# Optimization experiments

Hardware: AMD Instinct MI355X
Metric: run time of the kernel (lower is better)

## Reference

```python
import jax, jax.numpy as jnp
import numpy as np

N = 25600      # nodes
DEG = 16       # incoming edges per node
E = N * DEG    # 409600 edges
B = 8          # graphs in batch
F = 7          # node features
H = 300        # hidden_channels
L = 100        # latent_channels


def _mlp(h, W1, b1, W2, b2, W3, b3):
    h = jax.nn.relu(h @ W1 + b1)
    h = jax.nn.relu(h @ W2 + b2)
    return h @ W3 + b3


def _edge_layer(x, src, dst, params):
    # PyG MessagePassing(aggr='max'), flow source_to_target:
    # x_j = x[src] (edge_index[0]), x_i = x[dst] (edge_index[1])
    x_i = x[dst]
    x_j = x[src]
    m = _mlp(jnp.concatenate([x_i, x_j - x_i], axis=-1), *params)  # [E, out]
    # every node has >=1 incoming edge by construction, so no empty segments
    return jax.ops.segment_max(m, dst, num_segments=x.shape[0])


def setup_inputs() -> dict:
    key = jax.random.key(0)
    ks = jax.random.split(key, 24)
    x = jax.random.normal(ks[0], (N, F), jnp.float32)
    dst = jnp.repeat(jnp.arange(N, dtype=jnp.int32), DEG)          # every node covered
    src = jax.random.randint(ks[1], (E,), 0, N, dtype=jnp.int32)
    edge_index = jnp.stack([src, dst])                              # [2, E]
    batch = jnp.repeat(jnp.arange(B, dtype=jnp.int32), N // B)     # sorted graph ids

    def lin(k, i, o):
        return jax.random.normal(k, (i, o), jnp.float32) / jnp.sqrt(jnp.float32(i))

    def bias(k, o):
        return jax.random.normal(k, (o,), jnp.float32) * 0.01

    inp = dict(x=x, edge_index=edge_index, batch=batch)
    # layer 0 MLP: 2*F -> H -> H -> L
    inp.update(l0_W1=lin(ks[2], 2 * F, H), l0_b1=bias(ks[3], H),
               l0_W2=lin(ks[4], H, H),     l0_b2=bias(ks[5], H),
               l0_W3=lin(ks[6], H, L),     l0_b3=bias(ks[7], L))
    # layer 1 MLP: 2*L -> H -> H -> L
    inp.update(l1_W1=lin(ks[8], 2 * L, H), l1_b1=bias(ks[9], H),
               l1_W2=lin(ks[10], H, H),    l1_b2=bias(ks[11], H),
               l1_W3=lin(ks[12], H, L),    l1_b3=bias(ks[13], L))
    # final lin: 3*L -> L -> L -> 1
    inp.update(lin_W1=lin(ks[14], 3 * L, L), lin_b1=bias(ks[15], L),
               lin_W2=lin(ks[16], L, L),     lin_b2=bias(ks[17], L),
               lin_W3=lin(ks[18], L, 1),     lin_b3=bias(ks[19], 1))
    return inp


def reference(x, edge_index, batch,
              l0_W1, l0_b1, l0_W2, l0_b2, l0_W3, l0_b3,
              l1_W1, l1_b1, l1_W2, l1_b2, l1_W3, l1_b3,
              lin_W1, lin_b1, lin_W2, lin_b2, lin_W3, lin_b3):
    src, dst = edge_index[0], edge_index[1]
    h = _edge_layer(x, src, dst, (l0_W1, l0_b1, l0_W2, l0_b2, l0_W3, l0_b3))
    h = jax.nn.relu(h)
    h = _edge_layer(h, src, dst, (l1_W1, l1_b1, l1_W2, l1_b2, l1_W3, l1_b3))
    h = jax.nn.relu(h)                                              # [N, L]
    addp = jax.ops.segment_sum(h, batch, num_segments=B)
    cnt = jax.ops.segment_sum(jnp.ones((h.shape[0], 1), h.dtype), batch, num_segments=B)
    meanp = addp / cnt
    maxp = jax.ops.segment_max(h, batch, num_segments=B)
    pooled = jnp.concatenate([addp, meanp, maxp], axis=1)           # [B, 3L]
    return _mlp(pooled, lin_W1, lin_b1, lin_W2, lin_b2, lin_W3, lin_b3)  # [B, 1]
```

## Files before the change

kernel.cpp:

```cpp
#include <hip/hip_runtime.h>

#define NNODES 25600
#define DEG 16
#define BGRAPHS 8
#define NPG (NNODES / BGRAPHS)
#define FDIM 7
#define HDIM 300
#define LDIM 100
#define HP 320
#define UVW 640
#define NT1 20
#define KS1 10
#define NT2 7
#define KS2 10
#define H0W 128
#define SSTR 328

typedef __attribute__((ext_vector_type(8))) _Float16 half8;
typedef __attribute__((ext_vector_type(2))) _Float16 half2v;
typedef __attribute__((ext_vector_type(4))) float floatx4;

__device__ __forceinline__ unsigned short f2h(float f) {
    _Float16 h = (_Float16)f;
    return __builtin_bit_cast(unsigned short, h);
}

__device__ __forceinline__ half2v pkrtz(float a, float b) {
    return __builtin_bit_cast(half2v, __builtin_amdgcn_cvt_pkrtz(a, b));
}

union UV4H { uint4 v; half2v h[4]; };

__device__ __forceinline__ unsigned short packB(const float* W, int Kreal, int Nreal,
                                                int KS, int rel)
{
    int j = rel & 7, lane = (rel >> 3) & 63, rem = rel >> 9;
    int ks = rem % KS, nt = rem / KS;
    int k = ks * 32 + ((lane >> 4) << 3) + j;
    int n = nt * 16 + (lane & 15);
    float v = (k < Kreal && n < Nreal) ? W[k * Nreal + n] : 0.f;
    return f2h(v);
}

__device__ __forceinline__ unsigned short packProjW(const float* W1, int Ksub,
                                                    int KS, int rel)
{
    int j = rel & 7, lane = (rel >> 3) & 63, rem = rel >> 9;
    int ks = rem % KS, nt = rem / KS;
    int k = ks * 32 + ((lane >> 4) << 3) + j;
    int n = nt * 16 + (lane & 15);
    float v = 0.f;
    if (k < Ksub) {
        if (n < HP) { if (n < HDIM) v = W1[k * HDIM + n] - W1[(k + Ksub) * HDIM + n]; }
        else { int m = n - HP; if (m < HDIM) v = W1[(k + Ksub) * HDIM + m]; }
    }
    return f2h(v);
}

#define S0 102400
#define S1 102400
#define S2 35840
#define S3 35840
#define S4 81920
#define S5 20480
#define S6 1920
#define PACK_TOTAL (S0+S1+S2+S3+S4+S5+S6)

__global__ __launch_bounds__(256) void pack_all_kernel(
    const float* __restrict__ l0_W1, const float* __restrict__ l0_b1,
    const float* __restrict__ l0_W2, const float* __restrict__ l0_b2,
    const float* __restrict__ l0_W3,
    const float* __restrict__ l1_W1, const float* __restrict__ l1_b1,
    const float* __restrict__ l1_W2, const float* __restrict__ l1_b2,
    const float* __restrict__ l1_W3,
    unsigned short* __restrict__ PB2_0, unsigned short* __restrict__ PB2_1,
    unsigned short* __restrict__ PB3_0, unsigned short* __restrict__ PB3_1,
    unsigned short* __restrict__ PW1,  unsigned short* __restrict__ PW0,
    float* __restrict__ b2p_0, float* __restrict__ b2p_1,
    float* __restrict__ bp1,   float* __restrict__ bp0)
{
    int idx = blockIdx.x * 256 + threadIdx.x;
    if (idx >= PACK_TOTAL) return;
    if (idx < S0) { PB2_0[idx] = packB(l0_W2, HDIM, HDIM, KS1, idx); return; }
    idx -= S0;
    if (idx < S1) { PB2_1[idx] = packB(l1_W2, HDIM, HDIM, KS1, idx); return; }
    idx -= S1;
    if (idx < S2) { PB3_0[idx] = packB(l0_W3, HDIM, LDIM, KS2, idx); return; }
    idx -= S2;
    if (idx < S3) { PB3_1[idx] = packB(l1_W3, HDIM, LDIM, KS2, idx); return; }
    idx -= S3;
    if (idx < S4) { PW1[idx] = packProjW(l1_W1, LDIM, 4, idx); return; }
    idx -= S4;
    if (idx < S5) { PW0[idx] = packProjW(l0_W1, FDIM, 1, idx); return; }
    idx -= S5;
    if (idx < 320)       { b2p_0[idx] = (idx < HDIM) ? l0_b2[idx] : 0.f; return; }
    if (idx < 640)       { int n = idx - 320; b2p_1[n] = (n < HDIM) ? l1_b2[n] : 0.f; return; }
    if (idx < 1280)      { int n = idx - 640; bp1[n] = (n < HDIM) ? l1_b1[n] : 0.f; return; }
    { int n = idx - 1280; bp0[n] = (n < HDIM) ? l0_b1[n] : 0.f; }
}

template<int KS, bool A_IS_X>
__global__ __launch_bounds__(256) void proj_gemm_kernel(
    const void* __restrict__ Asrc, const unsigned short* __restrict__ PW,
    const float* __restrict__ bp,
    unsigned short* __restrict__ UV)
{
    __shared__ unsigned short As[4 * KS * 64 * 8];
    __shared__ unsigned short S[64 * SSTR];
    const int t = threadIdx.x;
    const int row0 = blockIdx.x * 64;

    if constexpr (A_IS_X) {
        const float* x = (const float*)Asrc;
        int lane = t & 63, mt = t >> 6;
        int quad = lane >> 4;
        int grow = row0 + mt * 16 + (lane & 15);
        unsigned short oz[8];
#pragma unroll
        for (int j = 0; j < 8; ++j) {
            int k = quad * 8 + j;
            oz[j] = (k < FDIM) ? f2h(x[grow * FDIM + k]) : (unsigned short)0;
        }
        *(uint4*)(As + t * 8) = *(uint4*)oz;
    } else {
        const unsigned short* h = (const unsigned short*)Asrc;
#pragma unroll
        for (int i = 0; i < 4; ++i) {
            int s = t + 256 * i;
            int lane = s & 63;
            int ks = (s >> 6) % KS;
            int mt = s / (KS * 64);
            int grow = row0 + mt * 16 + (lane & 15);
            int k0 = ks * 32 + ((lane >> 4) << 3);
            *(uint4*)(As + s * 8) = *(const uint4*)(h + (size_t)grow * H0W + k0);
        }
    }
    __syncthreads();

    const int w = t >> 6, lane = t & 63, quad = lane >> 4, l15 = lane & 15;

    for (int g = 0; g < 2; ++g) {
        const int ntb = g * 20 + w * 5;
        floatx4 c[5][4];
#pragma unroll
        for (int i = 0; i < 5; ++i)
#pragma unroll
            for (int mt = 0; mt < 4; ++mt) c[i][mt] = (floatx4){0.f, 0.f, 0.f, 0.f};
#pragma unroll
        for (int ks = 0; ks < KS; ++ks) {
            half8 a[4];
#pragma unroll
            for (int mt = 0; mt < 4; ++mt)
                a[mt] = *(const half8*)(As + ((mt * KS + ks) * 64 + lane) * 8);
#pragma unroll
            for (int i = 0; i < 5; ++i) {
                half8 b = *(const half8*)(PW + (size_t)(((ntb + i) * KS + ks) * 64 + lane) * 8);
#pragma unroll
                for (int mt = 0; mt < 4; ++mt)
                    c[i][mt] = __builtin_amdgcn_mfma_f32_16x16x32_f16(a[mt], b, c[i][mt], 0, 0, 0);
            }
        }
        __syncthreads();
#pragma unroll
        for (int i = 0; i < 5; ++i) {
            int colp = (w * 5 + i) * 16 + l15;
            float bb = bp[g * 320 + colp];
#pragma unroll
            for (int mt = 0; mt < 4; ++mt) {
#pragma unroll
                for (int r = 0; r < 4; ++r) {
                    int row = mt * 16 + quad * 4 + r;
                    S[row * SSTR + colp] = f2h(c[i][mt][r] + bb);
                }
            }
        }
        __syncthreads();
#pragma unroll
        for (int it = 0; it < 10; ++it) {
            int s = t + 256 * it;
            int row = s / 40, c4 = s - row * 40;
            uint4 v = *(const uint4*)(S + row * SSTR + c4 * 8);
            *(uint4*)(UV + (size_t)(row0 + row) * UVW + g * 320 + c4 * 8) = v;
        }
    }
}

template<bool OUT_HALF>
__global__ __launch_bounds__(512, 4) void edge_mfma_kernel(
    const unsigned short* __restrict__ UV,
    const int* __restrict__ src,
    const unsigned short* __restrict__ PB2, const float* __restrict__ b2p,
    const unsigned short* __restrict__ PB3, const float* __restrict__ b3,
    void* __restrict__ hout)
{
    __shared__ unsigned short Zs[4 * KS1 * 64 * 8];

    const int t = threadIdx.x;
    const int node0 = blockIdx.x * 4;
    const int lane = t & 63;
    const int w = t >> 6;
    const int quad = lane >> 4;
    const int l15 = lane & 15;
    const int slane = lane ^ ((lane & 0x30) >> 3);

    const int row16 = lane >> 2;
    const int part  = lane & 3;
    const int fl    = row16 + 16 * part;
    const int phys  = fl ^ (part << 1);

    const half2v hzero = {(_Float16)0.f, (_Float16)0.f};

#pragma unroll
    for (int i = 0; i < 5; ++i) {
        int s = t + 512 * i;
        int ks = (s >> 6) % KS1;
        int mt = s / (KS1 * 64);
        int m = mt * 16 + row16;
        int k0 = ks * 32 + part * 8;
        int srcn = src[node0 * 16 + m];
        UV4H ud, vd, o;
        ud.v = *(const uint4*)(UV + (size_t)(node0 + mt) * UVW + k0);
        vd.v = *(const uint4*)(UV + (size_t)srcn * UVW + HP + k0);
#pragma unroll
        for (int d = 0; d < 4; ++d) {
            half2v s2 = ud.h[d] + vd.h[d];
            o.h[d] = __builtin_elementwise_max(s2, hzero);
        }
        *(uint4*)(Zs + ((mt * KS1 + ks) * 64 + phys) * 8) = o.v;
    }
    __syncthreads();

    const int cnt1  = (w < 4) ? 3 : 2;
    const int base1 = (w < 4) ? 3 * w : 12 + 2 * (w - 4);
    floatx4 c1[3][4];
#pragma unroll
    for (int i = 0; i < 3; ++i)
#pragma unroll
        for (int mt = 0; mt < 4; ++mt) c1[i][mt] = (floatx4){0.f, 0.f, 0.f, 0.f};
    for (int ks = 0; ks < KS1; ++ks) {
        half8 zb[4];
#pragma unroll
        for (int mt = 0; mt < 4; ++mt)
            zb[mt] = *(const half8*)(Zs + ((mt * KS1 + ks) * 64 + slane) * 8);
#pragma unroll
        for (int i = 0; i < 3; ++i) {
            if (i < cnt1) {
                half8 wa = *(const half8*)(PB2 + (size_t)(((base1 + i) * KS1 + ks) * 64 + lane) * 8);
#pragma unroll
                for (int mt = 0; mt < 4; ++mt)
                    c1[i][mt] = __builtin_amdgcn_mfma_f32_16x16x32_f16(wa, zb[mt], c1[i][mt], 0, 0, 0);
            }
        }
    }
    __syncthreads();

#pragma unroll
    for (int i = 0; i < 3; ++i) {
        if (i < cnt1) {
            int B = base1 + i;
            const floatx4 bb = *(const floatx4*)(b2p + B * 16 + quad * 4);
            half2v hb0 = pkrtz(bb[0], bb[1]);
            half2v hb1 = pkrtz(bb[2], bb[3]);
            int ks = B >> 1;
            int khi = (2 * B + (quad >> 1)) & 3;
            int jo = (quad & 1) * 4;
#pragma unroll
            for (int mt = 0; mt < 4; ++mt) {
                half2v c01 = pkrtz(c1[i][mt][0], c1[i][mt][1]);
                half2v c23 = pkrtz(c1[i][mt][2], c1[i][mt][3]);
                union { half2v h[2]; unsigned long long ll; } o;
                o.h[0] = __builtin_elementwise_max(c01 + hb0, hzero);
                o.h[1] = __builtin_elementwise_max(c23 + hb1, hzero);
                *(unsigned long long*)(Zs + ((mt * KS1 + ks) * 64 + l15 + 16 * khi) * 8 + jo) = o.ll;
            }
        }
    }
    __syncthreads();

    floatx4 c2[4];
#pragma unroll
    for (int mt = 0; mt < 4; ++mt) c2[mt] = (floatx4){0.f, 0.f, 0.f, 0.f};
    if (w < NT2) {
        for (int ks = 0; ks < KS2; ++ks) {
            half8 a[4];
#pragma unroll
            for (int mt = 0; mt < 4; ++mt)
                a[mt] = *(const half8*)(Zs + ((mt * KS2 + ks) * 64 + lane) * 8);
            half8 b = *(const half8*)(PB3 + (size_t)((w * KS2 + ks) * 64 + lane) * 8);
#pragma unroll
            for (int mt = 0; mt < 4; ++mt)
                c2[mt] = __builtin_amdgcn_mfma_f32_16x16x32_f16(a[mt], b, c2[mt], 0, 0, 0);
        }
    }

#pragma unroll
    for (int mt = 0; mt < 4; ++mt) {
        int node = node0 + mt;
        if (w < NT2) {
            int col = w * 16 + l15;
            floatx4 a = c2[mt];
            float mx = fmaxf(fmaxf(a[0], a[1]), fmaxf(a[2], a[3]));
            mx = fmaxf(mx, __shfl_xor(mx, 16, 64));
            mx = fmaxf(mx, __shfl_xor(mx, 32, 64));
            if (quad == 0) {
                if (OUT_HALF) {
                    unsigned short val = 0;
                    if (col < LDIM) val = f2h(fmaxf(mx + b3[col], 0.f));
                    ((unsigned short*)hout)[(size_t)node * H0W + col] = val;
                } else {
                    if (col < LDIM)
                        ((float*)hout)[(size_t)node * LDIM + col] = fmaxf(mx + b3[col], 0.f);
                }
            }
        }
        if (OUT_HALF && w == 7 && quad == 0)
            ((unsigned short*)hout)[(size_t)node * H0W + 112 + l15] = 0;
    }
}

__global__ __launch_bounds__(128) void pool1_kernel(
    const float* __restrict__ h, float* __restrict__ part)
{
    int g = blockIdx.x / 25;
    int sl = blockIdx.x % 25;
    int t = threadIdx.x;
    int base = g * NPG + sl * 128;
    if (t < LDIM) {
        float s = 0.f, mx = -1e30f;
        for (int i = 0; i < 128; ++i) {
            float v = h[(size_t)(base + i) * LDIM + t];
            s += v;
            mx = fmaxf(mx, v);
        }
        part[(size_t)blockIdx.x * 200 + t] = s;
        part[(size_t)blockIdx.x * 200 + 100 + t] = mx;
    }
}

__global__ __launch_bounds__(256) void final_kernel(
    const float* __restrict__ part,
    const float* __restrict__ W1, const float* __restrict__ b1,
    const float* __restrict__ W2, const float* __restrict__ b2,
    const float* __restrict__ W3, const float* __restrict__ b3,
    float* __restrict__ out)
{
    __shared__ float P[BGRAPHS][3 * LDIM];
    __shared__ float T1[BGRAPHS][LDIM];
    __shared__ float T2[BGRAPHS][LDIM];
    int t = threadIdx.x;
    for (int i = t; i < BGRAPHS * LDIM; i += 256) {
        int g = i / LDIM, f = i - (i / LDIM) * LDIM;
        float s = 0.f, mx = -1e30f;
        for (int sl = 0; sl < 25; ++sl) {
            s += part[(size_t)(g * 25 + sl) * 200 + f];
            mx = fmaxf(mx, part[(size_t)(g * 25 + sl) * 200 + 100 + f]);
        }
        P[g][f] = s;
        P[g][LDIM + f] = s * (1.0f / NPG);
        P[g][2 * LDIM + f] = mx;
    }
    __syncthreads();
    for (int i = t; i < BGRAPHS * LDIM; i += 256) {
        int g = i / LDIM, c = i - (i / LDIM) * LDIM;
        float a = b1[c];
        for (int k = 0; k < 3 * LDIM; ++k) a = fmaf(P[g][k], W1[k * LDIM + c], a);
        T1[g][c] = fmaxf(a, 0.f);
    }
    __syncthreads();
    for (int i = t; i < BGRAPHS * LDIM; i += 256) {
        int g = i / LDIM, c = i - (i / LDIM) * LDIM;
        float a = b2[c];
        for (int k = 0; k < LDIM; ++k) a = fmaf(T1[g][k], W2[k * LDIM + c], a);
        T2[g][c] = fmaxf(a, 0.f);
    }
    __syncthreads();
    if (t < BGRAPHS) {
        float a = b3[0];
        for (int k = 0; k < LDIM; ++k) a = fmaf(T2[t][k], W3[k], a);
        out[t] = a;
    }
}

extern "C" void kernel_launch(void* const* d_in, const int* in_sizes, int n_in,
                              void* d_out, int out_size, void* d_ws, size_t ws_size,
                              hipStream_t stream)
{
    const float* x      = (const float*)d_in[0];
    const int*   src    = (const int*)d_in[1];
    const float* l0_W1  = (const float*)d_in[3];
    const float* l0_b1  = (const float*)d_in[4];
    const float* l0_W2  = (const float*)d_in[5];
    const float* l0_b2  = (const float*)d_in[6];
    const float* l0_W3  = (const float*)d_in[7];
    const float* l0_b3  = (const float*)d_in[8];
    const float* l1_W1  = (const float*)d_in[9];
    const float* l1_b1  = (const float*)d_in[10];
    const float* l1_W2  = (const float*)d_in[11];
    const float* l1_b2  = (const float*)d_in[12];
    const float* l1_W3  = (const float*)d_in[13];
    const float* l1_b3  = (const float*)d_in[14];
    const float* lin_W1 = (const float*)d_in[15];
    const float* lin_b1 = (const float*)d_in[16];
    const float* lin_W2 = (const float*)d_in[17];
    const float* lin_b2 = (const float*)d_in[18];
    const float* lin_W3 = (const float*)d_in[19];
    const float* lin_b3 = (const float*)d_in[20];
    float* out = (float*)d_out;

    char* p = (char*)d_ws;
    unsigned short* UV    = (unsigned short*)p;  p += (size_t)NNODES * UVW * 2;
    unsigned short* h0b   = (unsigned short*)p;  p += (size_t)NNODES * H0W * 2;
    float* h1             = (float*)p;           p += (size_t)NNODES * LDIM * 4;
    unsigned short* PB2_0 = (unsigned short*)p;  p += (size_t)S0 * 2;
    unsigned short* PB2_1 = (unsigned short*)p;  p += (size_t)S1 * 2;
    unsigned short* PB3_0 = (unsigned short*)p;  p += (size_t)S2 * 2;
    unsigned short* PB3_1 = (unsigned short*)p;  p += (size_t)S3 * 2;
    unsigned short* PW1   = (unsigned short*)p;  p += (size_t)S4 * 2;
    unsigned short* PW0   = (unsigned short*)p;  p += (size_t)S5 * 2;
    float* b2p_0          = (float*)p;           p += HP * 4;
    float* b2p_1          = (float*)p;           p += HP * 4;
    float* bp1            = (float*)p;           p += 640 * 4;
    float* bp0            = (float*)p;           p += 640 * 4;
    float* part           = (float*)p;           p += (size_t)200 * 200 * 4;

    pack_all_kernel<<<(PACK_TOTAL + 255) / 256, 256, 0, stream>>>(
        l0_W1, l0_b1, l0_W2, l0_b2, l0_W3,
        l1_W1, l1_b1, l1_W2, l1_b2, l1_W3,
        PB2_0, PB2_1, PB3_0, PB3_1, PW1, PW0, b2p_0, b2p_1, bp1, bp0);

    proj_gemm_kernel<1, true><<<NNODES / 64, 256, 0, stream>>>(x, PW0, bp0, UV);
    edge_mfma_kernel<true><<<NNODES / 4, 512, 0, stream>>>(UV, src, PB2_0, b2p_0, PB3_0, l0_b3, h0b);
    proj_gemm_kernel<4, false><<<NNODES / 64, 256, 0, stream>>>(h0b, PW1, bp1, UV);
    edge_mfma_kernel<false><<<NNODES / 4, 512, 0, stream>>>(UV, src, PB2_1, b2p_1, PB3_1, l1_b3, h1);
    pool1_kernel<<<200, 128, 0, stream>>>(h1, part);
    final_kernel<<<1, 256, 0, stream>>>(part, lin_W1, lin_b1, lin_W2, lin_b2, lin_W3, lin_b3, out);
}
```

Before: 428.1 us.

## Fuse graph pooling into second edge kernel via atomics; trim padded N-tile

The second edge-layer kernel now folds its per-node outputs straight into per-graph sum and max accumulators using atomicAdd and integer atomicMax. This removes the h1 buffer write, the pool1 kernel and the partial reduction in the final kernel. The accumulators are zeroed inside the pack kernel. It also cuts the second-GEMM N-tile count from 20 to 19, since columns beyond 300 are padding, and zeroes the corresponding shared-memory slab so the third GEMM still reads zeros. The risks are atomic contention on 1600 addresses and float-sum order nondeterminism. The integer-max trick relies on the values being non-negative after ReLU.

Result: slower. 448.1 us (+4.7%).

```diff
diff --git a/kernel.cpp b/kernel.cpp
--- a/kernel.cpp
+++ b/kernel.cpp
@@ -9,7 +9,7 @@
 #define LDIM 100
 #define HP 320
 #define UVW 640
-#define NT1 20
+#define NT1 19
 #define KS1 10
 #define NT2 7
 #define KS2 10
@@ -64,7 +64,8 @@
 #define S4 81920
 #define S5 20480
 #define S6 1920
-#define PACK_TOTAL (S0+S1+S2+S3+S4+S5+S6)
+#define S7 2048
+#define PACK_TOTAL (S0+S1+S2+S3+S4+S5+S6+S7)
 
 __global__ __launch_bounds__(256) void pack_all_kernel(
     const float* __restrict__ l0_W1, const float* __restrict__ l0_b1,
@@ -77,7 +78,8 @@
     unsigned short* __restrict__ PB3_0, unsigned short* __restrict__ PB3_1,
     unsigned short* __restrict__ PW1,  unsigned short* __restrict__ PW0,
     float* __restrict__ b2p_0, float* __restrict__ b2p_1,
-    float* __restrict__ bp1,   float* __restrict__ bp0)
+    float* __restrict__ bp1,   float* __restrict__ bp0,
+    float* __restrict__ part)
 {
     int idx = blockIdx.x * 256 + threadIdx.x;
     if (idx >= PACK_TOTAL) return;
@@ -96,7 +98,8 @@
     if (idx < 320)       { b2p_0[idx] = (idx < HDIM) ? l0_b2[idx] : 0.f; return; }
     if (idx < 640)       { int n = idx - 320; b2p_1[n] = (n < HDIM) ? l1_b2[n] : 0.f; return; }
     if (idx < 1280)      { int n = idx - 640; bp1[n] = (n < HDIM) ? l1_b1[n] : 0.f; return; }
-    { int n = idx - 1280; bp0[n] = (n < HDIM) ? l0_b1[n] : 0.f; }
+    if (idx < 1920)      { int n = idx - 1280; bp0[n] = (n < HDIM) ? l0_b1[n] : 0.f; return; }
+    part[idx - 1920] = 0.f;
 }
 
 template<int KS, bool A_IS_X>
@@ -230,8 +233,8 @@
     }
     __syncthreads();
 
-    const int cnt1  = (w < 4) ? 3 : 2;
-    const int base1 = (w < 4) ? 3 * w : 12 + 2 * (w - 4);
+    const int cnt1  = (w < 3) ? 3 : 2;
+    const int base1 = (w < 3) ? 3 * w : 9 + 2 * (w - 3);
     floatx4 c1[3][4];
 #pragma unroll
     for (int i = 0; i < 3; ++i)
@@ -275,6 +278,10 @@
             }
         }
     }
+    if (t < 128) {
+        int mt = t >> 5, ln = 32 + (t & 31);
+        *(uint4*)(Zs + ((mt * KS1 + 9) * 64 + ln) * 8) = (uint4){0u, 0u, 0u, 0u};
+    }
     __syncthreads();
 
     floatx4 c2[4];
@@ -293,47 +300,48 @@
         }
     }
 
-#pragma unroll
-    for (int mt = 0; mt < 4; ++mt) {
-        int node = node0 + mt;
-        if (w < NT2) {
-            int col = w * 16 + l15;
-            floatx4 a = c2[mt];
-            float mx = fmaxf(fmaxf(a[0], a[1]), fmaxf(a[2], a[3]));
-            mx = fmaxf(mx, __shfl_xor(mx, 16, 64));
-            mx = fmaxf(mx, __shfl_xor(mx, 32, 64));
-            if (quad == 0) {
-                if (OUT_HALF) {
+    if constexpr (OUT_HALF) {
+#pragma unroll
+        for (int mt = 0; mt < 4; ++mt) {
+            int node = node0 + mt;
+            if (w < NT2) {
+                int col = w * 16 + l15;
+                floatx4 a = c2[mt];
+                float mx = fmaxf(fmaxf(a[0], a[1]), fmaxf(a[2], a[3]));
+                mx = fmaxf(mx, __shfl_xor(mx, 16, 64));
+                mx = fmaxf(mx, __shfl_xor(mx, 32, 64));
+                if (quad == 0) {
                     unsigned short val = 0;
                     if (col < LDIM) val = f2h(fmaxf(mx + b3[col], 0.f));
                     ((unsigned short*)hout)[(size_t)node * H0W + col] = val;
-                } else {
-                    if (col < LDIM)
-                        ((float*)hout)[(size_t)node * LDIM + col] = fmaxf(mx + b3[col], 0.f);
                 }
             }
-        }
-        if (OUT_HALF && w == 7 && quad == 0)
-            ((unsigned short*)hout)[(size_t)node * H0W + 112 + l15] = 0;
-    }
-}
-
-__global__ __launch_bounds__(128) void pool1_kernel(
-    const float* __restrict__ h, float* __restrict__ part)
-{
-    int g = blockIdx.x / 25;
-    int sl = blockIdx.x % 25;
-    int t = threadIdx.x;
-    int base = g * NPG + sl * 128;
-    if (t < LDIM) {
-        float s = 0.f, mx = -1e30f;
-        for (int i = 0; i < 128; ++i) {
-            float v = h[(size_t)(base + i) * LDIM + t];
-            s += v;
-            mx = fmaxf(mx, v);
-        }
-        part[(size_t)blockIdx.x * 200 + t] = s;
-        part[(size_t)blockIdx.x * 200 + 100 + t] = mx;
+            if (w == 7 && quad == 0)
+                ((unsigned short*)hout)[(size_t)node * H0W + 112 + l15] = 0;
+        }
+    } else {
+        if (w < NT2) {
+            int col = w * 16 + l15;
+            float bv = (col < LDIM) ? b3[col] : 0.f;
+            float s4 = 0.f, m4 = 0.f;
+#pragma unroll
+            for (int mt = 0; mt < 4; ++mt) {
+                floatx4 a = c2[mt];
+                float mx = fmaxf(fmaxf(a[0], a[1]), fmaxf(a[2], a[3]));
+                mx = fmaxf(mx, __shfl_xor(mx, 16, 64));
+                mx = fmaxf(mx, __shfl_xor(mx, 32, 64));
+                float v = fmaxf(mx + bv, 0.f);
+                s4 += v;
+                m4 = fmaxf(m4, v);
+            }
+            if (quad == 0 && col < LDIM) {
+                int g = node0 / NPG;
+                float* ps = (float*)hout + g * 128 + col;
+                atomicAdd(ps, s4);
+                atomicMax((int*)((float*)hout + 1024 + g * 128 + col),
+                          __float_as_int(m4));
+            }
+        }
     }
 }
 
@@ -350,11 +358,8 @@
     int t = threadIdx.x;
     for (int i = t; i < BGRAPHS * LDIM; i += 256) {
         int g = i / LDIM, f = i - (i / LDIM) * LDIM;
-        float s = 0.f, mx = -1e30f;
-        for (int sl = 0; sl < 25; ++sl) {
-            s += part[(size_t)(g * 25 + sl) * 200 + f];
-            mx = fmaxf(mx, part[(size_t)(g * 25 + sl) * 200 + 100 + f]);
-        }
+        float s = part[g * 128 + f];
+        float mx = part[1024 + g * 128 + f];
         P[g][f] = s;
         P[g][LDIM + f] = s * (1.0f / NPG);
         P[g][2 * LDIM + f] = mx;
@@ -410,7 +415,6 @@
     char* p = (char*)d_ws;
     unsigned short* UV    = (unsigned short*)p;  p += (size_t)NNODES * UVW * 2;
     unsigned short* h0b   = (unsigned short*)p;  p += (size_t)NNODES * H0W * 2;
-    float* h1             = (float*)p;           p += (size_t)NNODES * LDIM * 4;
     unsigned short* PB2_0 = (unsigned short*)p;  p += (size_t)S0 * 2;
     unsigned short* PB2_1 = (unsigned short*)p;  p += (size_t)S1 * 2;
     unsigned short* PB3_0 = (unsigned short*)p;  p += (size_t)S2 * 2;
@@ -421,17 +425,16 @@
     float* b2p_1          = (float*)p;           p += HP * 4;
     float* bp1            = (float*)p;           p += 640 * 4;
     float* bp0            = (float*)p;           p += 640 * 4;
-    float* part           = (float*)p;           p += (size_t)200 * 200 * 4;
+    float* part           = (float*)p;           p += (size_t)2048 * 4;
 
     pack_all_kernel<<<(PACK_TOTAL + 255) / 256, 256, 0, stream>>>(
         l0_W1, l0_b1, l0_W2, l0_b2, l0_W3,
         l1_W1, l1_b1, l1_W2, l1_b2, l1_W3,
-        PB2_0, PB2_1, PB3_0, PB3_1, PW1, PW0, b2p_0, b2p_1, bp1, bp0);
+        PB2_0, PB2_1, PB3_0, PB3_1, PW1, PW0, b2p_0, b2p_1, bp1, bp0, part);
 
     proj_gemm_kernel<1, true><<<NNODES / 64, 256, 0, stream>>>(x, PW0, bp0, UV);
     edge_mfma_kernel<true><<<NNODES / 4, 512, 0, stream>>>(UV, src, PB2_0, b2p_0, PB3_0, l0_b3, h0b);
     proj_gemm_kernel<4, false><<<NNODES / 64, 256, 0, stream>>>(h0b, PW1, bp1, UV);
-    edge_mfma_kernel<false><<<NNODES / 4, 512, 0, stream>>>(UV, src, PB2_1, b2p_1, PB3_1, l1_b3, h1);
-    pool1_kernel<<<200, 128, 0, stream>>>(h1, part);
+    edge_mfma_kernel<false><<<NNODES / 4, 512, 0, stream>>>(UV, src, PB2_1, b2p_1, PB3_1, l1_b3, part);
     final_kernel<<<1, 256, 0, stream>>>(part, lin_W1, lin_b1, lin_W2, lin_b2, lin_W3, lin_b3, out);
 }
```
